# Optimization experiments

Hardware: AMD Instinct MI355X
Metric: run time of the kernel (lower is better)

The kernel has to match this reference:

```python
import jax, jax.numpy as jnp
import numpy as np

EPS = 1e-5

def mvn(x):
    # per-(N,C) spatial mean/std normalization; torch .var is unbiased (ddof=1)
    mean = jnp.mean(x, axis=(2, 3), keepdims=True)
    var = jnp.var(x, axis=(2, 3), ddof=1, keepdims=True)
    return (x - mean) / jnp.sqrt(var + EPS)

def conv1x1(x, w, b):
    # w: [O, C] (1x1 conv collapsed), x: [B, C, H, W]
    return jnp.einsum('bchw,oc->bohw', x, w) + b[None, :, None, None]

def conv3x3(x, w, b):
    # w: [O, I, 3, 3], VALID padding (snet uses padding=0)
    y = jax.lax.conv_general_dilated(x, w, (1, 1), 'VALID',
                                     dimension_numbers=('NCHW', 'OIHW', 'NCHW'))
    return y + b[None, :, None, None]

def safe_cbrt(x):
    # pow(relu(x), 1/3) with safe gradient at 0 (forward identical)
    pos = x > 0
    return jnp.where(pos, jnp.power(jnp.where(pos, x, 1.0), 1.0 / 3.0), 0.0)

def _forward(content, style, wf_san, bf_san, wg_san, bg_san, wh_san, bh_san,
             wf_mcc, bf_mcc, wg_mcc, bg_mcc, w_fc, b_fc, w_out, b_out,
             wc1, bc1, wc2, bc2, wc3, bc3, ws1, bs1, ws2, bs2, ws3, bs3,
             w_unc, b_unc):
    B, C, H, W = content.shape
    cn = mvn(content)
    sn = mvn(style)

    # --- MCC branch: channel correlation statistic of style ---
    F_Fc = conv1x1(cn, wf_mcc, bf_mcc)                      # [B,C,H,W]
    g = conv1x1(sn, wg_mcc, bg_mcc).reshape(B, C, H * W)    # [B,C,HW]
    FC_S = jnp.sum(g * g, axis=-1) / jnp.sum(g, axis=-1)    # [B,C]
    FC_S = FC_S @ w_fc.T + b_fc                             # Linear
    part1 = F_Fc * FC_S[:, :, None, None]

    # --- WCT-like covariance branch (compressed 32-dim space) ---
    Fs0 = style - jnp.mean(style, axis=(2, 3), keepdims=True)  # nor_mean
    fc_ = conv1x1(jax.nn.relu(conv1x1(jax.nn.relu(conv1x1(cn, wc1, bc1)), wc2, bc2)), wc3, bc3)  # [B,32,H,W]
    fs_ = conv1x1(jax.nn.relu(conv3x3(jax.nn.relu(conv3x3(Fs0, ws1, bs1)), ws2, bs2)), ws3, bs3)  # [B,32,H-4,W-4]
    cdim = fc_.shape[1]
    fs_flat = fs_.reshape(B, cdim, -1)                       # [B,32,hw_s]
    cov = jnp.einsum('bci,bdi->bcd', fs_flat, fs_flat) / fs_flat.shape[2]  # [B,32,32]
    out = jnp.einsum('bcd,bdi->bci', cov, fc_.reshape(B, cdim, H * W)).reshape(B, cdim, H, W)
    part2 = conv1x1(out, w_unc, b_unc)                       # [B,512,H,W]

    # --- SANet-style attention branch ---
    F_s = conv1x1(cn, wf_san, bf_san).reshape(B, C, H * W)
    G_s = conv1x1(sn, wg_san, bg_san).reshape(B, C, H * W)
    H_s = conv1x1(style, wh_san, bh_san).reshape(B, C, H * W)
    S = jax.nn.softmax(jnp.einsum('bci,bcj->bij', F_s, G_s), axis=-1)  # [B,HW,HW]
    part3 = jnp.einsum('bcj,bij->bci', H_s, S).reshape(B, C, H, W)

    p = safe_cbrt(jax.nn.relu(part1 * part2 * part3))
    return conv1x1(p, w_out, b_out) + content


def setup_inputs() -> dict:
    key = jax.random.key(0)
    B, C, H, W = 16, 512, 32, 32
    s = 0.02
    shapes = {
        'content': (B, C, H, W), 'style': (B, C, H, W),
        'wf_san': (C, C), 'bf_san': (C,), 'wg_san': (C, C), 'bg_san': (C,),
        'wh_san': (C, C), 'bh_san': (C,),
        'wf_mcc': (C, C), 'bf_mcc': (C,), 'wg_mcc': (C, C), 'bg_mcc': (C,),
        'w_fc': (C, C), 'b_fc': (C,), 'w_out': (C, C), 'b_out': (C,),
        'wc1': (256, 512), 'bc1': (256,), 'wc2': (128, 256), 'bc2': (128,),
        'wc3': (32, 128), 'bc3': (32,),
        'ws1': (256, 512, 3, 3), 'bs1': (256,), 'ws2': (128, 256, 3, 3), 'bs2': (128,),
        'ws3': (32, 128), 'bs3': (32,),
        'w_unc': (512, 32), 'b_unc': (512,),
    }
    d = {}
    for i, (name, shp) in enumerate(shapes.items()):
        k = jax.random.fold_in(key, i)
        scale = 1.0 if name in ('content', 'style') else s
        d[name] = jax.random.normal(k, shp, dtype=jnp.float32) * scale
    return d


def reference(content, style, wf_san, bf_san, wg_san, bg_san, wh_san, bh_san,
              wf_mcc, bf_mcc, wg_mcc, bg_mcc, w_fc, b_fc, w_out, b_out,
              wc1, bc1, wc2, bc2, wc3, bc3, ws1, bs1, ws2, bs2, ws3, bs3,
              w_unc, b_unc):
    return _forward(content, style, wf_san, bf_san, wg_san, bg_san, wh_san, bh_san,
                    wf_mcc, bf_mcc, wg_mcc, bg_mcc, w_fc, b_fc, w_out, b_out,
                    wc1, bc1, wc2, bc2, wc3, bc3, ws1, bs1, ws2, bs2, ws3, bs3,
                    w_unc, b_unc)
```

## Files before the change

kernel.cpp:

```cpp
#include <hip/hip_runtime.h>
#include <hip/hip_bf16.h>
#include <math.h>


typedef __attribute__((ext_vector_type(8))) short short8;
typedef __attribute__((ext_vector_type(4))) float f32x4;
typedef unsigned short us;
#define MFMA16 __builtin_amdgcn_mfma_f32_16x16x32_bf16

__device__ inline float b2f(us b) { return __uint_as_float(((unsigned)b) << 16); }
__device__ inline us f2b(float f) {
    unsigned u = __float_as_uint(f);
    return (us)((u + 0x7FFFu + ((u >> 16) & 1u)) >> 16);
}

__device__ inline double blockReduceSumD(double v, double* sh) {
    int t = threadIdx.x;
    sh[t] = v; __syncthreads();
    for (int s = blockDim.x >> 1; s > 0; s >>= 1) {
        if (t < s) sh[t] += sh[t + s];
        __syncthreads();
    }
    double r = sh[0]; __syncthreads();
    return r;
}

__global__ __launch_bounds__(256) void stats_k(const float* __restrict__ X,
                                               float* __restrict__ mean,
                                               float* __restrict__ inv, int HW) {
    __shared__ double sh[256];
    int bc = blockIdx.x;
    const float* x = X + (size_t)bc * HW;
    int t = threadIdx.x;
    float v[4];
    double s = 0.0;
    #pragma unroll
    for (int r = 0; r < 4; ++r) { v[r] = x[t + r * 256]; s += (double)v[r]; }
    double tot = blockReduceSumD(s, sh);
    double ss = 0.0;
    #pragma unroll
    for (int r = 0; r < 4; ++r) ss += (double)v[r] * (double)v[r];
    double tot2 = blockReduceSumD(ss, sh);
    if (t == 0) {
        double m = tot / HW;
        double var = (tot2 - tot * tot / HW) / (HW - 1);
        mean[bc] = (float)m;
        inv[bc] = (float)(1.0 / sqrt(var + 1e-5));
    }
}

__global__ __launch_bounds__(256) void trn_k(const float* __restrict__ X,
                                             const float* __restrict__ mean,
                                             const float* __restrict__ inv,
                                             us* __restrict__ Yn, us* __restrict__ Yc,
                                             us* __restrict__ Yr, int C, int HW) {
    __shared__ us Ln[64 * 65];
    __shared__ us Lc[64 * 65];
    __shared__ us Lr[64 * 65];
    int bz = blockIdx.z, c0 = blockIdx.y * 64, h0 = blockIdx.x * 64;
    const float* Xb = X + (size_t)bz * C * HW;
    int t = threadIdx.x;
    int cl = t >> 3, h8 = (t & 7) * 8;
    #pragma unroll
    for (int half = 0; half < 2; ++half) {
        int c = cl + half * 32;
        int gc = c0 + c;
        float m = mean[bz * C + gc], iv = inv[bz * C + gc];
        const float4* s4 = (const float4*)&Xb[(size_t)gc * HW + h0 + h8];
        float4 f0 = s4[0], f1 = s4[1];
        float vv[8] = {f0.x, f0.y, f0.z, f0.w, f1.x, f1.y, f1.z, f1.w};
        #pragma unroll
        for (int i = 0; i < 8; ++i) {
            int li = c * 65 + h8 + i;
            if (Yn) Ln[li] = f2b((vv[i] - m) * iv);
            if (Yc) Lc[li] = f2b(vv[i] - m);
            if (Yr) Lr[li] = f2b(vv[i]);
        }
    }
    __syncthreads();
    int hl = t >> 3, c8 = (t & 7) * 8;
    #pragma unroll
    for (int half = 0; half < 2; ++half) {
        int hh = hl + half * 32;
        size_t off = ((size_t)bz * HW + h0 + hh) * (size_t)C + c0 + c8;
        us tmp[8];
        if (Yn) {
            #pragma unroll
            for (int i = 0; i < 8; ++i) tmp[i] = Ln[(c8 + i) * 65 + hh];
            *(uint4*)&Yn[off] = *(const uint4*)tmp;
        }
        if (Yc) {
            #pragma unroll
            for (int i = 0; i < 8; ++i) tmp[i] = Lc[(c8 + i) * 65 + hh];
            *(uint4*)&Yc[off] = *(const uint4*)tmp;
        }
        if (Yr) {
            #pragma unroll
            for (int i = 0; i < 8; ++i) tmp[i] = Lr[(c8 + i) * 65 + hh];
            *(uint4*)&Yr[off] = *(const uint4*)tmp;
        }
    }
}

template <typename TE>
__device__ inline void stage16(const TE* __restrict__ src, bool valid, us* dst) {
    us tmp[16];
    if (valid) {
        if constexpr (sizeof(TE) == 2) {
            uint4 a = ((const uint4*)src)[0], b = ((const uint4*)src)[1];
            *(uint4*)&tmp[0] = a; *(uint4*)&tmp[8] = b;
        } else {
            const float4* s4 = (const float4*)src;
            float4 f0 = s4[0], f1 = s4[1], f2 = s4[2], f3 = s4[3];
            float vv[16] = {f0.x, f0.y, f0.z, f0.w, f1.x, f1.y, f1.z, f1.w,
                            f2.x, f2.y, f2.z, f2.w, f3.x, f3.y, f3.z, f3.w};
            #pragma unroll
            for (int i = 0; i < 16; ++i) tmp[i] = f2b(vv[i]);
        }
    } else {
        #pragma unroll
        for (int i = 0; i < 16; ++i) tmp[i] = 0;
    }
    ((uint4*)dst)[0] = *(uint4*)&tmp[0];
    ((uint4*)dst)[1] = *(uint4*)&tmp[8];
}

template <typename TAel, typename TBel, typename TOUT, int OUTT>
__global__ __launch_bounds__(256) void mf2_k(const TAel* __restrict__ A, long astride, int lda,
                                             const TBel* __restrict__ B, long bstride, int ldb,
                                             const float* __restrict__ bias,
                                             TOUT* __restrict__ Y,
                                             const float* __restrict__ add_src,
                                             int K, int M, int N, int relu) {
    __shared__ us As[128][40];
    __shared__ us Bs[128][40];
    int bz = blockIdx.z;
    int mbase = blockIdx.y * 128, nbase = blockIdx.x * 128;
    const TAel* Ab = A + (size_t)bz * astride;
    const TBel* Bb = B + (size_t)bz * bstride;
    int t = threadIdx.x;
    int row = t & 127, kh = t >> 7;
    int wave = t >> 6, lane = t & 63, lm = lane & 15, q = lane >> 4;
    int mh = (wave >> 1) * 64, nh = (wave & 1) * 64;

    f32x4 acc[4][4];
    #pragma unroll
    for (int i = 0; i < 4; ++i)
        #pragma unroll
        for (int j = 0; j < 4; ++j) acc[i][j] = (f32x4){0.f, 0.f, 0.f, 0.f};

    for (int kb = 0; kb < K; kb += 32) {
        int gm = mbase + row;
        stage16(Ab + (size_t)gm * lda + kb + kh * 16, gm < M, &As[row][kh * 16]);
        int gn = nbase + row;
        stage16(Bb + (size_t)gn * ldb + kb + kh * 16, gn < N, &Bs[row][kh * 16]);
        __syncthreads();
        short8 af[4], bf[4];
        #pragma unroll
        for (int i = 0; i < 4; ++i) af[i] = *(const short8*)&As[mh + i * 16 + lm][q * 8];
        #pragma unroll
        for (int j = 0; j < 4; ++j) bf[j] = *(const short8*)&Bs[nh + j * 16 + lm][q * 8];
        #pragma unroll
        for (int i = 0; i < 4; ++i)
            #pragma unroll
            for (int j = 0; j < 4; ++j)
                acc[i][j] = MFMA16(af[i], bf[j], acc[i][j], 0, 0, 0);
        __syncthreads();
    }

    #pragma unroll
    for (int i = 0; i < 4; ++i) {
        int m0 = mbase + mh + i * 16 + q * 4;
        if (m0 >= M) continue;
        float bv[4];
        #pragma unroll
        for (int r = 0; r < 4; ++r) bv[r] = bias ? bias[m0 + r] : 0.f;
        #pragma unroll
        for (int j = 0; j < 4; ++j) {
            int n = nbase + nh + j * 16 + lm;
            if (n >= N) continue;
            float v[4];
            #pragma unroll
            for (int r = 0; r < 4; ++r) {
                float x = acc[i][j][r] + bv[r];
                if (relu) x = (x > 0.f) ? x : 0.f;
                v[r] = x;
            }
            if (OUTT == 1) {
                size_t off = ((size_t)bz * N + n) * (size_t)M + m0;
                if constexpr (sizeof(TOUT) == 2) {
                    us o4[4];
                    #pragma unroll
                    for (int r = 0; r < 4; ++r) o4[r] = f2b(v[r]);
                    *(uint2*)&Y[off] = *(const uint2*)o4;
                } else {
                    float4 f4 = make_float4(v[0], v[1], v[2], v[3]);
                    *(float4*)&Y[off] = f4;
                }
            } else {
                #pragma unroll
                for (int r = 0; r < 4; ++r) {
                    size_t off = ((size_t)bz * M + m0 + r) * (size_t)N + n;
                    float x = v[r];
                    if (add_src) x += add_src[off];
                    if constexpr (sizeof(TOUT) == 2) Y[off] = f2b(x);
                    else Y[off] = x;
                }
            }
        }
    }
}

__global__ __launch_bounds__(256) void reorder_wf_k(const float* __restrict__ W,
                                                    us* __restrict__ Wf, int O, int Cin) {
    int idx = blockIdx.x * 256 + threadIdx.x;
    int OT = O >> 6, KB = Cin >> 5;
    int total = OT * KB * 9 * 4 * 64;
    if (idx >= total) return;
    int lane = idx & 63;
    int f = idx >> 6;
    int i = f & 1, half = (f >> 1) & 1;
    int tf = f >> 2;
    int tap = tf % 9;
    int rest = tf / 9;
    int kb = rest % KB, ot = rest / KB;
    int o = ot * 64 + half * 32 + i * 16 + (lane & 15);
    int cb = kb * 32 + (lane >> 4) * 8;
    us v[8];
    #pragma unroll
    for (int e = 0; e < 8; ++e)
        v[e] = f2b(W[((size_t)o * Cin + cb + e) * 9 + tap]);
    *(uint4*)&Wf[(size_t)idx * 8] = *(const uint4*)v;
}

template <int PR>
__global__ __launch_bounds__(256) void conv_mf3_k(const us* __restrict__ X, long xbstride,
                                                  const us* __restrict__ Wf,
                                                  const float* __restrict__ bias,
                                                  us* __restrict__ Y, long ybstride,
                                                  int Cin, int O, int IH, int IW,
                                                  int OH, int OW) {
    __shared__ us patch[(2 * PR + 2) * 36 * 40];
    int bz = blockIdx.z;
    int obase = blockIdx.y * 64;
    int pyb = blockIdx.x * (2 * PR);
    const us* Xb = X + (size_t)bz * xbstride;
    int t = threadIdx.x;
    int wave = t >> 6, lane = t & 63, lm = lane & 15, q = lane >> 4;
    int half = wave >> 1, rw = wave & 1;
    int KB = Cin >> 5;
    const us* Wb = Wf + (size_t)(obase >> 6) * KB * 9 * 2048;

    f32x4 acc[PR][2][2];
    #pragma unroll
    for (int pr = 0; pr < PR; ++pr)
        #pragma unroll
        for (int i = 0; i < 2; ++i)
            #pragma unroll
            for (int j = 0; j < 2; ++j) acc[pr][i][j] = (f32x4){0.f, 0.f, 0.f, 0.f};

    const int ITEMS = (2 * PR + 2) * 36 * 4;
    for (int kb = 0; kb < KB; ++kb) {
        __syncthreads();
        for (int i = t; i < ITEMS; i += 256) {
            int p = i >> 2, q8 = (i & 3) * 8;
            int r = p / 36, x = p - r * 36;
            int gy = pyb + r;
            uint4 v = make_uint4(0u, 0u, 0u, 0u);
            if (x < IW && gy < IH)
                v = *(const uint4*)&Xb[((size_t)(gy * IW + x)) * Cin + kb * 32 + q8];
            *(uint4*)&patch[p * 40 + q8] = v;
        }
        __syncthreads();
        const us* Wk = Wb + (size_t)kb * 9 * 2048;
        #pragma unroll
        for (int tap = 0; tap < 9; ++tap) {
            int ky = tap / 3, kx = tap - ky * 3;
            const us* wt = Wk + tap * 2048 + half * 1024;
            short8 a0 = *(const short8*)&wt[lane * 8];
            short8 a1 = *(const short8*)&wt[512 + lane * 8];
            #pragma unroll
            for (int pr = 0; pr < PR; ++pr) {
                int prow = (pr * 2 + rw + ky) * 36;
                short8 b0 = *(const short8*)&patch[(prow + lm + kx) * 40 + q * 8];
                short8 b1 = *(const short8*)&patch[(prow + 16 + lm + kx) * 40 + q * 8];
                acc[pr][0][0] = MFMA16(a0, b0, acc[pr][0][0], 0, 0, 0);
                acc[pr][0][1] = MFMA16(a0, b1, acc[pr][0][1], 0, 0, 0);
                acc[pr][1][0] = MFMA16(a1, b0, acc[pr][1][0], 0, 0, 0);
                acc[pr][1][1] = MFMA16(a1, b1, acc[pr][1][1], 0, 0, 0);
            }
        }
    }

    us* Yb = Y + (size_t)bz * ybstride;
    #pragma unroll
    for (int pr = 0; pr < PR; ++pr) {
        int py = pyb + pr * 2 + rw;
        if (py >= OH) continue;
        #pragma unroll
        for (int i = 0; i < 2; ++i) {
            int m0 = obase + half * 32 + i * 16 + q * 4;
            #pragma unroll
            for (int j = 0; j < 2; ++j) {
                int px = j * 16 + lm;
                if (px >= OW) continue;
                us o4[4];
                #pragma unroll
                for (int r = 0; r < 4; ++r) {
                    float v = acc[pr][i][j][r] + bias[m0 + r];
                    v = (v > 0.f) ? v : 0.f;
                    o4[r] = f2b(v);
                }
                *(uint2*)&Yb[((size_t)(py * OW + px)) * O + m0] = *(const uint2*)o4;
            }
        }
    }
}

__global__ __launch_bounds__(256) void gemm_k(const float* __restrict__ W,
                                              const float* __restrict__ X,
                                              const float* __restrict__ bias,
                                              float* __restrict__ Y,
                                              int C, int O, int N) {
    int obase = blockIdx.y * 32;
    __shared__ float As[32][33];
    __shared__ float Bs[32][33];
    int t = threadIdx.x;
    int tx = t & 15, ty = t >> 4;
    float acc00 = 0, acc01 = 0, acc10 = 0, acc11 = 0;
    for (int cb = 0; cb < C; cb += 32) {
        int k = t & 31, o0 = t >> 5;
        #pragma unroll
        for (int r = 0; r < 4; ++r) {
            int ol = o0 + r * 8;
            As[k][ol] = W[(size_t)(obase + ol) * C + cb + k];
        }
        int n0 = t & 31, k0 = t >> 5;
        #pragma unroll
        for (int r = 0; r < 4; ++r) {
            int k2 = k0 + r * 8;
            Bs[k2][n0] = (n0 < N) ? X[(size_t)(cb + k2) * N + n0] : 0.f;
        }
        __syncthreads();
        #pragma unroll
        for (int k2 = 0; k2 < 32; ++k2) {
            float a0 = As[k2][ty], a1 = As[k2][ty + 16];
            float b0 = Bs[k2][tx], b1 = Bs[k2][tx + 16];
            acc00 += a0 * b0; acc01 += a0 * b1;
            acc10 += a1 * b0; acc11 += a1 * b1;
        }
        __syncthreads();
    }
    float accs[2][2] = {{acc00, acc01}, {acc10, acc11}};
    #pragma unroll
    for (int i = 0; i < 2; ++i) {
        int o = obase + ty + i * 16;
        float bv = bias[o];
        #pragma unroll
        for (int j = 0; j < 2; ++j) {
            int n = tx + j * 16;
            if (n < N) Y[(size_t)o * N + n] = accs[i][j] + bv;
        }
    }
}

__global__ __launch_bounds__(256) void fcs2_k(const us* __restrict__ g,
                                              const float* __restrict__ bg,
                                              float* __restrict__ fcs,
                                              int HW, int B, int C) {
    __shared__ double sh[256];
    int bc = blockIdx.x;
    int b = bc / C, c = bc - b * C;
    const us* x = g + (size_t)bc * HW;
    int t = threadIdx.x;
    uint2 v = *(const uint2*)&x[t * 4];
    us u[4]; *(uint2*)u = v;
    double ss = 0.0;
    #pragma unroll
    for (int i = 0; i < 4; ++i) { double gv = (double)b2f(u[i]); ss += gv * gv; }
    double tss = blockReduceSumD(ss, sh);
    if (t == 0) fcs[(size_t)c * B + b] = (float)(tss / ((double)HW * (double)bg[c]));
}

__global__ __launch_bounds__(256) void softmax_k(const float* __restrict__ S,
                                                 us* __restrict__ P) {
    __shared__ float sh[256];
    size_t row = blockIdx.x;
    const float* r = S + row * 1024;
    us* po = P + row * 1024;
    int t = threadIdx.x;
    float v[4];
    float m = -INFINITY;
    #pragma unroll
    for (int i = 0; i < 4; ++i) { v[i] = r[t + i * 256]; m = fmaxf(m, v[i]); }
    sh[t] = m; __syncthreads();
    for (int s = 128; s > 0; s >>= 1) { if (t < s) sh[t] = fmaxf(sh[t], sh[t + s]); __syncthreads(); }
    m = sh[0]; __syncthreads();
    float sum = 0;
    #pragma unroll
    for (int i = 0; i < 4; ++i) { v[i] = expf(v[i] - m); sum += v[i]; }
    sh[t] = sum; __syncthreads();
    for (int s = 128; s > 0; s >>= 1) { if (t < s) sh[t] += sh[t + s]; __syncthreads(); }
    float inv = 1.f / sh[0]; __syncthreads();
    #pragma unroll
    for (int i = 0; i < 4; ++i) po[t + i * 256] = f2b(v[i] * inv);
}

__global__ __launch_bounds__(256) void cov2_k(const float* __restrict__ fs,
                                              float* __restrict__ cov, int Cd, int M) {
    __shared__ float Ls[196 * 36];
    int bb = blockIdx.x;
    int t = threadIdx.x;
    const float* p = fs + (size_t)bb * M * Cd;
    int c = t >> 3, d0 = (t & 7) * 4;
    float a0 = 0.f, a1 = 0.f, a2 = 0.f, a3 = 0.f;
    for (int ch = 0; ch < 4; ++ch) {
        __syncthreads();
        for (int i = t; i < 1568; i += 256) {
            int rowi = i >> 3, c4 = (i & 7) * 4;
            float4 v = *(const float4*)&p[(size_t)(ch * 196 + rowi) * Cd + c4];
            *(float4*)&Ls[rowi * 36 + c4] = v;
        }
        __syncthreads();
        for (int i = 0; i < 196; ++i) {
            float a = Ls[i * 36 + c];
            a0 += a * Ls[i * 36 + d0 + 0];
            a1 += a * Ls[i * 36 + d0 + 1];
            a2 += a * Ls[i * 36 + d0 + 2];
            a3 += a * Ls[i * 36 + d0 + 3];
        }
    }
    float invM = 1.f / (float)M;
    size_t base = ((size_t)bb * Cd + c) * Cd + d0;
    cov[base + 0] = a0 * invM;
    cov[base + 1] = a1 * invM;
    cov[base + 2] = a2 * invM;
    cov[base + 3] = a3 * invM;
}

__global__ __launch_bounds__(256) void fuse_k(const us* __restrict__ ffc,
                                              const float* __restrict__ fc2t,
                                              const us* __restrict__ p2,
                                              const us* __restrict__ p3,
                                              us* __restrict__ out, int B, int C, int HW) {
    size_t idx = (size_t)blockIdx.x * 256 + threadIdx.x;
    size_t total = (size_t)B * C * HW;
    if (idx >= total) return;
    int c = (int)(idx & (size_t)(C - 1));
    int b = (int)(idx / ((size_t)C * HW));
    float part1 = b2f(ffc[idx]) * fc2t[(size_t)c * B + b];
    float v = part1 * b2f(p2[idx]) * b2f(p3[idx]);
    v = (v > 0.f) ? v : 0.f;
    out[idx] = f2b(cbrtf(v));
}

extern "C" void kernel_launch(void* const* d_in, const int* in_sizes, int n_in,
                              void* d_out, int out_size, void* d_ws, size_t ws_size,
                              hipStream_t stream) {
    typedef const float* fp;
    fp content = (fp)d_in[0];
    fp style   = (fp)d_in[1];
    fp wf_san = (fp)d_in[2],  bf_san = (fp)d_in[3];
    fp wg_san = (fp)d_in[4],  bg_san = (fp)d_in[5];
    fp wh_san = (fp)d_in[6],  bh_san = (fp)d_in[7];
    fp wf_mcc = (fp)d_in[8],  bf_mcc = (fp)d_in[9];
    fp wg_mcc = (fp)d_in[10], bg_mcc = (fp)d_in[11];
    fp w_fc   = (fp)d_in[12], b_fc   = (fp)d_in[13];
    fp w_out  = (fp)d_in[14], b_out  = (fp)d_in[15];
    fp wc1 = (fp)d_in[16], bc1 = (fp)d_in[17];
    fp wc2 = (fp)d_in[18], bc2 = (fp)d_in[19];
    fp wc3 = (fp)d_in[20], bc3 = (fp)d_in[21];
    fp ws1 = (fp)d_in[22], bs1 = (fp)d_in[23];
    fp ws2 = (fp)d_in[24], bs2 = (fp)d_in[25];
    fp ws3 = (fp)d_in[26], bs3 = (fp)d_in[27];
    fp w_unc = (fp)d_in[28], b_unc = (fp)d_in[29];

    const int B = 16, C = 512, HW = 1024;
    const size_t NE = (size_t)B * C * HW;
    const long TOK = (long)C * HW;
    char* base = (char*)d_ws;
    const size_t SL = 16777216;

    us* gbuf  = (us*)(base + 0 * SL);
    float* Sbuf  = (float*)(base + 0 * SL);
    us* fs0T  = (us*)(base + 3 * SL);
    us* cnT   = (us*)(base + 4 * SL);
    us* snT   = (us*)(base + 5 * SL);
    us* Pb    = (us*)(base + 4 * SL);
    us* styleT = (us*)(base + 6 * SL);
    us* ffcb  = (us*)(base + 7 * SL);
    us* Fsb   = (us*)(base + 8 * SL);
    us* Gsb   = (us*)(base + 9 * SL);
    us* part2 = (us*)(base + 10 * SL);
    us* t1 = (us*)(base + 11 * SL);
    us* t2 = (us*)(base + 11 * SL + 8388608);
    us* s1 = (us*)(base + 12 * SL);
    us* s2 = (us*)(base + 12 * SL + 7372800);
    us* part3 = Fsb;
    us* Hco   = Gsb;
    us* pbuf  = ffcb;

    char* misc = base + 13 * SL;
    us* Wr1 = (us*)(misc);
    us* Wr2 = (us*)(misc + 2359296);
    float* fc_c  = (float*)(misc + 2949120);
    float* fs_c  = (float*)(misc + 5046272);
    float* out32 = (float*)(misc + 6651904);
    float* fcs   = (float*)(misc + 8749056);
    float* fc2t  = (float*)(misc + 8781824);
    float* cov   = (float*)(misc + 8814592);
    float* meanC = (float*)(misc + 8880128);
    float* invC  = (float*)(misc + 8912896);
    float* meanS = (float*)(misc + 8945664);
    float* invS  = (float*)(misc + 8978432);

    reorder_wf_k<<<576, 256, 0, stream>>>(ws1, Wr1, 256, 512);
    reorder_wf_k<<<72, 256, 0, stream>>>(ws2, Wr2, 128, 256);

    stats_k<<<B * C, 256, 0, stream>>>(content, meanC, invC, HW);
    stats_k<<<B * C, 256, 0, stream>>>(style, meanS, invS, HW);
    trn_k<<<dim3(16, 8, 16), 256, 0, stream>>>(content, meanC, invC, cnT, nullptr, nullptr, C, HW);
    trn_k<<<dim3(16, 8, 16), 256, 0, stream>>>(style, meanS, invS, snT, fs0T, styleT, C, HW);

    mf2_k<float, us, us, 0><<<dim3(8, 4, 16), 256, 0, stream>>>(
        wg_mcc, 0, 512, snT, TOK, 512, bg_mcc, gbuf, nullptr, 512, 512, 1024, 0);
    fcs2_k<<<B * C, 256, 0, stream>>>(gbuf, bg_mcc, fcs, HW, B, C);
    gemm_k<<<dim3(1, 16, 1), 256, 0, stream>>>(w_fc, fcs, b_fc, fc2t, 512, 512, 16);

    mf2_k<float, us, us, 1><<<dim3(8, 4, 16), 256, 0, stream>>>(
        wf_mcc, 0, 512, cnT, TOK, 512, bf_mcc, ffcb, nullptr, 512, 512, 1024, 0);

    mf2_k<float, us, us, 1><<<dim3(8, 2, 16), 256, 0, stream>>>(
        wc1, 0, 512, cnT, TOK, 512, bc1, t1, nullptr, 512, 256, 1024, 1);
    mf2_k<float, us, us, 1><<<dim3(8, 1, 16), 256, 0, stream>>>(
        wc2, 0, 256, t1, (long)1024 * 256, 256, bc2, t2, nullptr, 256, 128, 1024, 1);
    mf2_k<float, us, float, 1><<<dim3(8, 1, 16), 256, 0, stream>>>(
        wc3, 0, 128, t2, (long)1024 * 128, 128, bc3, fc_c, nullptr, 128, 32, 1024, 0);

    conv_mf3_k<2><<<dim3(8, 4, 16), 256, 0, stream>>>(fs0T, TOK, Wr1, bs1,
                                                      s1, (long)900 * 256, 512, 256, 32, 32, 30, 30);
    conv_mf3_k<1><<<dim3(14, 2, 16), 256, 0, stream>>>(s1, (long)900 * 256, Wr2, bs2,
                                                       s2, (long)784 * 128, 256, 128, 30, 30, 28, 28);
    mf2_k<float, us, float, 1><<<dim3(7, 1, 16), 256, 0, stream>>>(
        ws3, 0, 128, s2, (long)784 * 128, 128, bs3, fs_c, nullptr, 128, 32, 784, 0);

    cov2_k<<<B, 256, 0, stream>>>(fs_c, cov, 32, 784);
    mf2_k<float, float, float, 1><<<dim3(8, 1, 16), 256, 0, stream>>>(
        cov, 1024, 32, fc_c, (long)1024 * 32, 32, nullptr, out32, nullptr, 32, 32, 1024, 0);
    mf2_k<float, float, us, 1><<<dim3(8, 4, 16), 256, 0, stream>>>(
        w_unc, 0, 32, out32, (long)1024 * 32, 32, b_unc, part2, nullptr, 32, 512, 1024, 0);

    mf2_k<float, us, us, 1><<<dim3(8, 4, 16), 256, 0, stream>>>(
        wf_san, 0, 512, cnT, TOK, 512, bf_san, Fsb, nullptr, 512, 512, 1024, 0);
    mf2_k<float, us, us, 1><<<dim3(8, 4, 16), 256, 0, stream>>>(
        wg_san, 0, 512, snT, TOK, 512, bg_san, Gsb, nullptr, 512, 512, 1024, 0);

    mf2_k<us, us, float, 0><<<dim3(8, 8, 16), 256, 0, stream>>>(
        Fsb, TOK, 512, Gsb, TOK, 512, nullptr, Sbuf, nullptr, 512, 1024, 1024, 0);
    softmax_k<<<B * HW, 256, 0, stream>>>(Sbuf, Pb);

    mf2_k<float, us, us, 0><<<dim3(8, 4, 16), 256, 0, stream>>>(
        wh_san, 0, 512, styleT, TOK, 512, bh_san, Hco, nullptr, 512, 512, 1024, 0);

    mf2_k<us, us, us, 0><<<dim3(4, 8, 16), 256, 0, stream>>>(
        Pb, (long)1024 * 1024, 1024, Hco, TOK, 1024, nullptr, part3, nullptr, 1024, 1024, 512, 0);

    fuse_k<<<(unsigned)((NE + 255) / 256), 256, 0, stream>>>(ffcb, fc2t, part2, part3, pbuf, B, C, HW);

    mf2_k<float, us, float, 0><<<dim3(8, 4, 16), 256, 0, stream>>>(
        w_out, 0, 512, pbuf, TOK, 512, b_out, (float*)d_out, content, 512, 512, 1024, 0);
}
```

Measured before the change: 898.5 us.

## Batch 1x1 conv GEMMs sharing an input into stacked-weight MFMA kernels

Result: faster. 879.6 us (-2.1%).

```diff
diff --git a/kernel.cpp b/kernel.cpp
--- a/kernel.cpp
+++ b/kernel.cpp
@@ -211,6 +211,83 @@
     }
 }
 
+struct SBias {
+    const float* bp[10];
+    int moff[10];
+    unsigned relu;
+};
+__global__ __launch_bounds__(256) void mfs_k(const us* __restrict__ A,
+                                             const us* __restrict__ B, long bstride, int ldb,
+                                             us* __restrict__ Y, int ldy,
+                                             SBias sb, int K, int N) {
+    __shared__ us As[128][40];
+    __shared__ us Bs[128][40];
+    int bz = blockIdx.z;
+    int mbase = blockIdx.y * 128, nbase = blockIdx.x * 128;
+    const us* Bb = B + (size_t)bz * bstride;
+    int t = threadIdx.x;
+    int row = t & 127, kh = t >> 7;
+    int wave = t >> 6, lane = t & 63, lm = lane & 15, q = lane >> 4;
+    int mh = (wave >> 1) * 64, nh = (wave & 1) * 64;
+    int relu = (sb.relu >> blockIdx.y) & 1;
+    const float* bias = sb.bp[blockIdx.y];
+    int moff = sb.moff[blockIdx.y];
+
+    f32x4 acc[4][4];
+    #pragma unroll
+    for (int i = 0; i < 4; ++i)
+        #pragma unroll
+        for (int j = 0; j < 4; ++j) acc[i][j] = (f32x4){0.f, 0.f, 0.f, 0.f};
+
+    for (int kb = 0; kb < K; kb += 32) {
+        stage16(A + (size_t)(mbase + row) * K + kb + kh * 16, true, &As[row][kh * 16]);
+        stage16(Bb + (size_t)(nbase + row) * ldb + kb + kh * 16, true, &Bs[row][kh * 16]);
+        __syncthreads();
+        short8 af[4], bf[4];
+        #pragma unroll
+        for (int i = 0; i < 4; ++i) af[i] = *(const short8*)&As[mh + i * 16 + lm][q * 8];
+        #pragma unroll
+        for (int j = 0; j < 4; ++j) bf[j] = *(const short8*)&Bs[nh + j * 16 + lm][q * 8];
+        #pragma unroll
+        for (int i = 0; i < 4; ++i)
+            #pragma unroll
+            for (int j = 0; j < 4; ++j)
+                acc[i][j] = MFMA16(af[i], bf[j], acc[i][j], 0, 0, 0);
+        __syncthreads();
+    }
+
+    #pragma unroll
+    for (int i = 0; i < 4; ++i) {
+        int m0 = mbase + mh + i * 16 + q * 4;
+        float bv[4];
+        #pragma unroll
+        for (int r = 0; r < 4; ++r) bv[r] = bias[m0 - moff + r];
+        #pragma unroll
+        for (int j = 0; j < 4; ++j) {
+            int n = nbase + nh + j * 16 + lm;
+            us o4[4];
+            #pragma unroll
+            for (int r = 0; r < 4; ++r) {
+                float x = acc[i][j][r] + bv[r];
+                if (relu) x = (x > 0.f) ? x : 0.f;
+                o4[r] = f2b(x);
+            }
+            *(uint2*)&Y[((size_t)bz * N + n) * ldy + m0] = *(const uint2*)o4;
+        }
+    }
+}
+
+struct CpyArg {
+    const float* src[11];
+    unsigned long long dstoff[11];
+    int len[11];
+};
+__global__ __launch_bounds__(256) void wcat_k(CpyArg a, us* __restrict__ arena) {
+    int seg = blockIdx.y;
+    int idx = blockIdx.x * 256 + threadIdx.x;
+    if (idx < a.len[seg]) arena[a.dstoff[seg] + idx] = f2b(a.src[seg][idx]);
+}
+
 __global__ __launch_bounds__(256) void reorder_wf_k(const float* __restrict__ W,
                                                     us* __restrict__ Wf, int O, int Cin) {
     int idx = blockIdx.x * 256 + threadIdx.x;
@@ -364,22 +441,25 @@
     }
 }
 
-__global__ __launch_bounds__(256) void fcs2_k(const us* __restrict__ g,
+__global__ __launch_bounds__(256) void fcs3_k(const us* __restrict__ g, int ldg,
                                               const float* __restrict__ bg,
                                               float* __restrict__ fcs,
-                                              int HW, int B, int C) {
-    __shared__ double sh[256];
-    int bc = blockIdx.x;
-    int b = bc / C, c = bc - b * C;
-    const us* x = g + (size_t)bc * HW;
-    int t = threadIdx.x;
-    uint2 v = *(const uint2*)&x[t * 4];
-    us u[4]; *(uint2*)u = v;
-    double ss = 0.0;
-    #pragma unroll
-    for (int i = 0; i < 4; ++i) { double gv = (double)b2f(u[i]); ss += gv * gv; }
-    double tss = blockReduceSumD(ss, sh);
-    if (t == 0) fcs[(size_t)c * B + b] = (float)(tss / ((double)HW * (double)bg[c]));
+                                              int B, int HW) {
+    int b = blockIdx.x;
+    int t = threadIdx.x;
+    const us* gb = g + (size_t)b * HW * ldg + 2 * t;
+    double s0 = 0.0, s1 = 0.0;
+    #pragma unroll 4
+    for (int hw = 0; hw < HW; ++hw) {
+        unsigned u = *(const unsigned*)&gb[(size_t)hw * ldg];
+        float f0 = b2f((us)(u & 0xFFFFu));
+        float f1 = b2f((us)(u >> 16));
+        s0 += (double)f0 * (double)f0;
+        s1 += (double)f1 * (double)f1;
+    }
+    int c0 = 2 * t;
+    fcs[(size_t)c0 * B + b] = (float)(s0 / ((double)HW * (double)bg[c0]));
+    fcs[(size_t)(c0 + 1) * B + b] = (float)(s1 / ((double)HW * (double)bg[c0 + 1]));
 }
 
 __global__ __launch_bounds__(256) void softmax_k(const float* __restrict__ S,
@@ -438,7 +518,7 @@
     cov[base + 3] = a3 * invM;
 }
 
-__global__ __launch_bounds__(256) void fuse_k(const us* __restrict__ ffc,
+__global__ __launch_bounds__(256) void fuse_k(const us* __restrict__ ffc, int ldf,
                                               const float* __restrict__ fc2t,
                                               const us* __restrict__ p2,
                                               const us* __restrict__ p3,
@@ -447,8 +527,9 @@
     size_t total = (size_t)B * C * HW;
     if (idx >= total) return;
     int c = (int)(idx & (size_t)(C - 1));
+    size_t tok = idx >> 9;
     int b = (int)(idx / ((size_t)C * HW));
-    float part1 = b2f(ffc[idx]) * fc2t[(size_t)c * B + b];
+    float part1 = b2f(ffc[tok * ldf + c]) * fc2t[(size_t)c * B + b];
     float v = part1 * b2f(p2[idx]) * b2f(p3[idx]);
     v = (v > 0.f) ? v : 0.f;
     out[idx] = f2b(cbrtf(v));
@@ -478,42 +559,55 @@
     const int B = 16, C = 512, HW = 1024;
     const size_t NE = (size_t)B * C * HW;
     const long TOK = (long)C * HW;
+    const size_t MB = 1u << 20;
     char* base = (char*)d_ws;
-    const size_t SL = 16777216;
-
-    us* gbuf  = (us*)(base + 0 * SL);
-    float* Sbuf  = (float*)(base + 0 * SL);
-    us* fs0T  = (us*)(base + 3 * SL);
-    us* cnT   = (us*)(base + 4 * SL);
-    us* snT   = (us*)(base + 5 * SL);
-    us* Pb    = (us*)(base + 4 * SL);
-    us* styleT = (us*)(base + 6 * SL);
-    us* ffcb  = (us*)(base + 7 * SL);
-    us* Fsb   = (us*)(base + 8 * SL);
-    us* Gsb   = (us*)(base + 9 * SL);
-    us* part2 = (us*)(base + 10 * SL);
-    us* t1 = (us*)(base + 11 * SL);
-    us* t2 = (us*)(base + 11 * SL + 8388608);
-    us* s1 = (us*)(base + 12 * SL);
-    us* s2 = (us*)(base + 12 * SL + 7372800);
-    us* part3 = Fsb;
-    us* Hco   = Gsb;
-    us* pbuf  = ffcb;
-
-    char* misc = base + 13 * SL;
-    us* Wr1 = (us*)(misc);
-    us* Wr2 = (us*)(misc + 2359296);
-    float* fc_c  = (float*)(misc + 2949120);
-    float* fs_c  = (float*)(misc + 5046272);
-    float* out32 = (float*)(misc + 6651904);
-    float* fcs   = (float*)(misc + 8749056);
-    float* fc2t  = (float*)(misc + 8781824);
-    float* cov   = (float*)(misc + 8814592);
-    float* meanC = (float*)(misc + 8880128);
-    float* invC  = (float*)(misc + 8912896);
-    float* meanS = (float*)(misc + 8945664);
-    float* invS  = (float*)(misc + 8978432);
-
+
+    float* Sbuf  = (float*)(base);
+    us* cnT      = (us*)(base);
+    us* snT      = (us*)(base + 16 * MB);
+    us* Hco      = (us*)(base + 32 * MB);
+    us* t2b      = (us*)(base);
+    float* fc_c  = (float*)(base + 4 * MB);
+    float* fs_c  = (float*)(base + 6 * MB);
+    float* out32 = (float*)(base + 8 * MB);
+    us* cnOut    = (us*)(base + 64 * MB);
+    us* snOut    = (us*)(base + 104 * MB);
+    us* part3b   = (us*)(base + 104 * MB);
+    us* pbuf     = (us*)(base + 120 * MB);
+    us* Pb       = (us*)(base + 136 * MB);
+    us* part2b   = (us*)(base + 136 * MB);
+    us* fs0T     = (us*)(base + 168 * MB);
+    us* styleT   = (us*)(base + 184 * MB);
+    us* s1       = (us*)(base + 184 * MB);
+    us* s2       = (us*)(base + 192 * MB);
+
+    char* misc = base + 200 * MB;
+    us* Wr1   = (us*)(misc);
+    us* Wr2   = (us*)(misc + 2359296);
+    us* Wcn   = (us*)(misc + 2949120);
+    us* Wsn   = (us*)(misc + 4259840);
+    us* Wh    = (us*)(misc + 5308416);
+    us* Wout  = (us*)(misc + 5832704);
+    us* Wc2   = (us*)(misc + 6356992);
+    us* Wc3   = (us*)(misc + 6422528);
+    us* Ws3   = (us*)(misc + 6430720);
+    us* Wunc  = (us*)(misc + 6438912);
+    float* fcs   = (float*)(misc + 6471680);
+    float* fc2t  = (float*)(misc + 6504448);
+    float* cov   = (float*)(misc + 6537216);
+    float* meanC = (float*)(misc + 6602752);
+    float* invC  = (float*)(misc + 6635520);
+    float* meanS = (float*)(misc + 6668288);
+    float* invS  = (float*)(misc + 6701056);
+
+    CpyArg ca;
+    const float* srcs[11] = {wf_mcc, wc1, wf_san, wg_mcc, wg_san, wh_san,
+                             w_out, wc2, wc3, ws3, w_unc};
+    int lens[11] = {262144, 131072, 262144, 262144, 262144, 262144,
+                    262144, 32768, 4096, 4096, 16384};
+    unsigned long long off = 0;
+    for (int i = 0; i < 11; ++i) { ca.src[i] = srcs[i]; ca.dstoff[i] = off; ca.len[i] = lens[i]; off += lens[i]; }
+    wcat_k<<<dim3(1024, 11), 256, 0, stream>>>(ca, Wcn);
     reorder_wf_k<<<576, 256, 0, stream>>>(ws1, Wr1, 256, 512);
     reorder_wf_k<<<72, 256, 0, stream>>>(ws2, Wr2, 128, 256);
 
@@ -522,51 +616,59 @@
     trn_k<<<dim3(16, 8, 16), 256, 0, stream>>>(content, meanC, invC, cnT, nullptr, nullptr, C, HW);
     trn_k<<<dim3(16, 8, 16), 256, 0, stream>>>(style, meanS, invS, snT, fs0T, styleT, C, HW);
 
-    mf2_k<float, us, us, 0><<<dim3(8, 4, 16), 256, 0, stream>>>(
-        wg_mcc, 0, 512, snT, TOK, 512, bg_mcc, gbuf, nullptr, 512, 512, 1024, 0);
-    fcs2_k<<<B * C, 256, 0, stream>>>(gbuf, bg_mcc, fcs, HW, B, C);
+    {
+        SBias sb;
+        for (int y = 0; y < 4; ++y) { sb.bp[y] = bf_mcc; sb.moff[y] = 0; }
+        for (int y = 4; y < 6; ++y) { sb.bp[y] = bc1; sb.moff[y] = 512; }
+        for (int y = 6; y < 10; ++y) { sb.bp[y] = bf_san; sb.moff[y] = 768; }
+        sb.relu = 0x030u;
+        mfs_k<<<dim3(8, 10, 16), 256, 0, stream>>>(Wcn, cnT, TOK, 512, cnOut, 1280, sb, 512, 1024);
+    }
+
+    {
+        SBias sb;
+        for (int y = 0; y < 4; ++y) { sb.bp[y] = bg_mcc; sb.moff[y] = 0; }
+        for (int y = 4; y < 8; ++y) { sb.bp[y] = bg_san; sb.moff[y] = 512; }
+        for (int y = 8; y < 10; ++y) { sb.bp[y] = bg_mcc; sb.moff[y] = 0; }
+        sb.relu = 0u;
+        mfs_k<<<dim3(8, 8, 16), 256, 0, stream>>>(Wsn, snT, TOK, 512, snOut, 1024, sb, 512, 1024);
+    }
+
+    fcs3_k<<<B, 256, 0, stream>>>(snOut, 1024, bg_mcc, fcs, B, HW);
     gemm_k<<<dim3(1, 16, 1), 256, 0, stream>>>(w_fc, fcs, b_fc, fc2t, 512, 512, 16);
 
-    mf2_k<float, us, us, 1><<<dim3(8, 4, 16), 256, 0, stream>>>(
-        wf_mcc, 0, 512, cnT, TOK, 512, bf_mcc, ffcb, nullptr, 512, 512, 1024, 0);
-
-    mf2_k<float, us, us, 1><<<dim3(8, 2, 16), 256, 0, stream>>>(
-        wc1, 0, 512, cnT, TOK, 512, bc1, t1, nullptr, 512, 256, 1024, 1);
-    mf2_k<float, us, us, 1><<<dim3(8, 1, 16), 256, 0, stream>>>(
-        wc2, 0, 256, t1, (long)1024 * 256, 256, bc2, t2, nullptr, 256, 128, 1024, 1);
-    mf2_k<float, us, float, 1><<<dim3(8, 1, 16), 256, 0, stream>>>(
-        wc3, 0, 128, t2, (long)1024 * 128, 128, bc3, fc_c, nullptr, 128, 32, 1024, 0);
+    mf2_k<us, us, float, 0><<<dim3(8, 8, 16), 256, 0, stream>>>(
+        cnOut + 768, (long)1024 * 1280, 1280, snOut + 512, (long)1024 * 1024, 1024,
+        nullptr, Sbuf, nullptr, 512, 1024, 1024, 0);
+    softmax_k<<<B * HW, 256, 0, stream>>>(Sbuf, Pb);
+
+    mf2_k<us, us, us, 0><<<dim3(8, 4, 16), 256, 0, stream>>>(
+        Wh, 0, 512, styleT, TOK, 512, bh_san, Hco, nullptr, 512, 512, 1024, 0);
+
+    mf2_k<us, us, us, 0><<<dim3(4, 8, 16), 256, 0, stream>>>(
+        Pb, (long)1024 * 1024, 1024, Hco, TOK, 1024, nullptr, part3b, nullptr, 1024, 1024, 512, 0);
+
+    mf2_k<us, us, us, 1><<<dim3(8, 1, 16), 256, 0, stream>>>(
+        Wc2, 0, 256, cnOut + 512, (long)1024 * 1280, 1280, bc2, t2b, nullptr, 256, 128, 1024, 1);
+    mf2_k<us, us, float, 1><<<dim3(8, 1, 16), 256, 0, stream>>>(
+        Wc3, 0, 128, t2b, (long)1024 * 128, 128, bc3, fc_c, nullptr, 128, 32, 1024, 0);
 
     conv_mf3_k<2><<<dim3(8, 4, 16), 256, 0, stream>>>(fs0T, TOK, Wr1, bs1,
                                                       s1, (long)900 * 256, 512, 256, 32, 32, 30, 30);
     conv_mf3_k<1><<<dim3(14, 2, 16), 256, 0, stream>>>(s1, (long)900 * 256, Wr2, bs2,
                                                        s2, (long)784 * 128, 256, 128, 30, 30, 28, 28);
-    mf2_k<float, us, float, 1><<<dim3(7, 1, 16), 256, 0, stream>>>(
-        ws3, 0, 128, s2, (long)784 * 128, 128, bs3, fs_c, nullptr, 128, 32, 784, 0);
+    mf2_k<us, us, float, 1><<<dim3(7, 1, 16), 256, 0, stream>>>(
+        Ws3, 0, 128, s2, (long)784 * 128, 128, bs3, fs_c, nullptr, 128, 32, 784, 0);
 
     cov2_k<<<B, 256, 0, stream>>>(fs_c, cov, 32, 784);
     mf2_k<float, float, float, 1><<<dim3(8, 1, 16), 256, 0, stream>>>(
         cov, 1024, 32, fc_c, (long)1024 * 32, 32, nullptr, out32, nullptr, 32, 32, 1024, 0);
-    mf2_k<float, float, us, 1><<<dim3(8, 4, 16), 256, 0, stream>>>(
-        w_unc, 0, 32, out32, (long)1024 * 32, 32, b_unc, part2, nullptr, 32, 512, 1024, 0);
-
-    mf2_k<float, us, us, 1><<<dim3(8, 4, 16), 256, 0, stream>>>(
-        wf_san, 0, 512, cnT, TOK, 512, bf_san, Fsb, nullptr, 512, 512, 1024, 0);
-    mf2_k<float, us, us, 1><<<dim3(8, 4, 16), 256, 0, stream>>>(
-        wg_san, 0, 512, snT, TOK, 512, bg_san, Gsb, nullptr, 512, 512, 1024, 0);
-
-    mf2_k<us, us, float, 0><<<dim3(8, 8, 16), 256, 0, stream>>>(
-        Fsb, TOK, 512, Gsb, TOK, 512, nullptr, Sbuf, nullptr, 512, 1024, 1024, 0);
-    softmax_k<<<B * HW, 256, 0, stream>>>(Sbuf, Pb);
-
-    mf2_k<float, us, us, 0><<<dim3(8, 4, 16), 256, 0, stream>>>(
-        wh_san, 0, 512, styleT, TOK, 512, bh_san, Hco, nullptr, 512, 512, 1024, 0);
-
-    mf2_k<us, us, us, 0><<<dim3(4, 8, 16), 256, 0, stream>>>(
-        Pb, (long)1024 * 1024, 1024, Hco, TOK, 1024, nullptr, part3, nullptr, 1024, 1024, 512, 0);
-
-    fuse_k<<<(unsigned)((NE + 255) / 256), 256, 0, stream>>>(ffcb, fc2t, part2, part3, pbuf, B, C, HW);
-
-    mf2_k<float, us, float, 0><<<dim3(8, 4, 16), 256, 0, stream>>>(
-        w_out, 0, 512, pbuf, TOK, 512, b_out, (float*)d_out, content, 512, 512, 1024, 0);
-}
+    mf2_k<us, float, us, 1><<<dim3(8, 4, 16), 256, 0, stream>>>(
+        Wunc, 0, 32, out32, (long)1024 * 32, 32, b_unc, part2b, nullptr, 32, 512, 1024, 0);
+
+    fuse_k<<<(unsigned)((NE + 255) / 256), 256, 0, stream>>>(
+        cnOut, 1280, fc2t, part2b, part3b, pbuf, B, C, HW);
+
+    mf2_k<us, us, float, 0><<<dim3(8, 4, 16), 256, 0, stream>>>(
+        Wout, 0, 512, pbuf, TOK, 512, b_out, (float*)d_out, content, 512, 512, 1024, 0);
+}
```
